# Kernel tuning notes

Measured on AMD Instinct MI355X. Metric: run time of the kernel, lower is better.

Reference implementation:

```python
import jax, jax.numpy as jnp
import numpy as np

N = 65536          # nodes
K = 12             # graph_k
CHUNK = 1024       # graph_knn_chunk (capped at 1024 in source)
WIDTH = 256        # mlp width
GWIDTH = 192       # graph width
DEPTH = 7          # mlp depth
GLAYERS = 4        # graph layers
COND = 64          # cond_dim
NUM_FF = 8         # fourier num per sigma
SIGMAS = (1.0, 10.0, 50.0)
SKIPS = (3, 6)     # residual skips
OUT_SCALE = 0.01
FF_DIM = 2 * len(SIGMAS) * NUM_FF  # 48 (sin+cos per sigma band)


def fourier_feats(x, B):
    # x: (N,3), B: (S,3,NUM_FF) -> (N, 2*S*NUM_FF)
    proj = jnp.einsum('nd,sdm->nsm', x, B).reshape(x.shape[0], -1)
    return jnp.concatenate([jnp.sin(proj), jnp.cos(proj)], axis=-1)


def knn_graph(x):
    # chunked exact kNN: mirrors _build_knn_graph (chunked cdist + top-k)
    x_sq = jnp.sum(x * x, axis=1)  # (N,)
    n = x.shape[0]
    col_ids = jnp.arange(n)

    def chunk_fn(start):
        rows = start + jnp.arange(CHUNK)
        xc = x[rows]                                   # (C,3)
        d = x_sq[rows][:, None] + x_sq[None, :] - 2.0 * (xc @ x.T)  # (C,N)
        d = jnp.maximum(d, 0.0)
        d = d + jnp.where(rows[:, None] == col_ids[None, :], 1e9, 0.0)  # exclude self
        _, idx = jax.lax.top_k(-d, K)                  # k smallest distances
        return idx

    idx = jax.lax.map(chunk_fn, jnp.arange(0, n, CHUNK))  # (n/C, C, K)
    return idx.reshape(n, K)


def setup_inputs() -> dict:
    key = jax.random.key(0)
    ks = jax.random.split(key, 16)
    g = lambda k, shape, fan: jax.random.normal(k, shape, jnp.float32) / np.sqrt(fan)
    sig = jnp.asarray(SIGMAS, jnp.float32)[:, None, None]
    return {
        'x': jax.random.normal(ks[0], (N, 3), jnp.float32),
        'cond': jax.random.normal(ks[1], (COND,), jnp.float32),
        'B': jax.random.normal(ks[2], (len(SIGMAS), 3, NUM_FF), jnp.float32) * sig,
        'W_in': g(ks[3], (FF_DIM, WIDTH), FF_DIM),
        'b_in': jnp.zeros((WIDTH,), jnp.float32),
        'Wg_in': g(ks[4], (FF_DIM, GWIDTH), FF_DIM),
        'bg_in': jnp.zeros((GWIDTH,), jnp.float32),
        'Ws': g(ks[5], (GLAYERS, GWIDTH, GWIDTH), GWIDTH),
        'Wn': g(ks[6], (GLAYERS, GWIDTH, GWIDTH), GWIDTH),
        'bg': jnp.zeros((GLAYERS, GWIDTH), jnp.float32),
        'Wg_out': g(ks[7], (GWIDTH, WIDTH), GWIDTH),
        'W': g(ks[8], (DEPTH, WIDTH, WIDTH), WIDTH),
        'bmlp': jnp.zeros((DEPTH, WIDTH), jnp.float32),
        'Wf_g': g(ks[9], (DEPTH, COND, WIDTH), COND),
        'bf_g': jnp.zeros((DEPTH, WIDTH), jnp.float32),
        'Wf_b': g(ks[10], (DEPTH, COND, WIDTH), COND),
        'bf_b': jnp.zeros((DEPTH, WIDTH), jnp.float32),
        'W_out': g(ks[11], (WIDTH, 3), WIDTH),
        'b_out': jnp.zeros((3,), jnp.float32),
    }


def reference(x, cond, B, W_in, b_in, Wg_in, bg_in, Ws, Wn, bg, Wg_out,
              W, bmlp, Wf_g, bf_g, Wf_b, bf_b, W_out, b_out):
    act = jax.nn.silu
    knn_idx = knn_graph(x)                     # (N,K) graph structure
    ff = fourier_feats(x, B)                   # (N,48)
    h0 = act(ff @ W_in + b_in)                 # (N,256) coordinate embedding

    # graph message-passing branch (row-normalized 1/K adjacency == neighbor mean)
    gfeat = act(ff @ Wg_in + bg_in)            # (N,192)
    for l in range(GLAYERS):
        agg = jnp.mean(gfeat[knn_idx], axis=1)  # sparse spmm: gather + mean
        gfeat = act(gfeat @ Ws[l] + agg @ Wn[l] + bg[l])

    h = h0 + gfeat @ Wg_out                    # inject graph context

    # FiLM-conditioned residual MLP trunk
    for l in range(DEPTH):
        gamma = cond @ Wf_g[l] + bf_g[l]       # (256,)
        beta = cond @ Wf_b[l] + bf_b[l]
        h = act((h @ W[l] + bmlp[l]) * (1.0 + gamma) + beta)
        if (l + 1) in SKIPS:
            h = h + h0

    return (h @ W_out + b_out) * OUT_SCALE     # (N,3) displacement
```

## Files before the change

kernel.cpp:

```cpp
#include <hip/hip_runtime.h>
#include <math.h>

#define NN      65536
#define KNN     12
#define WIDTH   256
#define GW      192
#define DEPTH   7
#define GLAYERS 4
#define FF      48

#define GC    192
#define GC3   7077888
#define GLO   (-6.0f)
#define GCW   0.0625f
#define GINV  16.0f

#define GS     128
#define GS3    2097152
#define GSINV  10.666666667f
#define CS2    0.09375f

#define QL    16

#define RT2   0.2025f

typedef __attribute__((ext_vector_type(8))) _Float16 half8;
typedef __attribute__((ext_vector_type(4))) _Float16 half4;
typedef __attribute__((ext_vector_type(4))) float    f4;

__device__ __forceinline__ float silu_f(float v) { return v / (1.0f + expf(-v)); }

#define KSWAP(A,B,IA,IB) do { if (B < A) { float _t=A; A=B; B=_t; int _u=IA; IA=IB; IB=_u; } } while(0)
#define KINSERT(DV,IV) do { b11=(DV); j11=(IV); \
    KSWAP(b10,b11,j10,j11); KSWAP(b9,b10,j9,j10); KSWAP(b8,b9,j8,j9); \
    KSWAP(b7,b8,j7,j8);  KSWAP(b6,b7,j6,j7);  KSWAP(b5,b6,j5,j6); \
    KSWAP(b4,b5,j4,j5);  KSWAP(b3,b4,j3,j4);  KSWAP(b2,b3,j2,j3); \
    KSWAP(b1,b2,j1,j2);  KSWAP(b0,b1,j0,j1); } while(0)

__device__ __forceinline__ int cell_of(float v) {
    int c = (int)floorf((v - GLO) * GINV);
    return min(max(c, 0), GC-1);
}

__device__ __forceinline__ int cell2(float v) {
    int c = (int)floorf((v - GLO) * GSINV);
    return min(max(c, 0), GS-1);
}

__global__ __launch_bounds__(256) void zero_both_kernel(int* __restrict__ cnt,
                                                        int* __restrict__ cnt2,
                                                        int* __restrict__ octr) {
    int g = blockIdx.x*256 + threadIdx.x;
    if (g == 0) { octr[0] = 0; octr[1] = 0; octr[2] = 0; }
    if (g < GC3/4) *(int4*)&cnt[g*4] = make_int4(0,0,0,0);
    else           *(int4*)&cnt2[(g - GC3/4)*4] = make_int4(0,0,0,0);
}

__global__ __launch_bounds__(256) void prep_hist_kernel(const float* __restrict__ x,
                                                        float4* __restrict__ xw,
                                                        int* __restrict__ cnt,
                                                        int* __restrict__ cnt2) {
    int i = blockIdx.x*256 + threadIdx.x;
    float a = x[3*i], b = x[3*i+1], c = x[3*i+2];
    xw[i] = make_float4(a, b, c, a*a + b*b + c*c);
    atomicAdd(&cnt[(cell_of(c)*GC + cell_of(b))*GC + cell_of(a)], 1);
    atomicAdd(&cnt2[(cell2(c)*GS + cell2(b))*GS + cell2(a)], 1);
}

__global__ __launch_bounds__(256) void satx_kernel(int* __restrict__ S) {
    const int wid  = (blockIdx.x*256 + threadIdx.x) >> 6;
    const int lane = threadIdx.x & 63;
    const int base = wid * GC;
    int carry = 0;
#pragma unroll
    for (int seg = 0; seg < 3; ++seg) {
        int v = S[base + seg*64 + lane];
#pragma unroll
        for (int off = 1; off < 64; off <<= 1) {
            int n = __shfl_up(v, off);
            if (lane >= off) v += n;
        }
        v += carry;
        S[base + seg*64 + lane] = v;
        carry = __shfl(v, 63);
    }
}

__global__ __launch_bounds__(256) void saty_kernel(int* __restrict__ S) {
    int t = blockIdx.x*256 + threadIdx.x;
    int z = t / GC, xx = t % GC, run = 0;
    for (int y = 0; y < GC; ++y) { int idx = (z*GC + y)*GC + xx; run += S[idx]; S[idx] = run; }
}
__global__ __launch_bounds__(256) void satz_kernel(int* __restrict__ S) {
    int t = blockIdx.x*256 + threadIdx.x;
    int y = t / GC, xx = t % GC, run = 0;
    for (int z = 0; z < GC; ++z) { int idx = (z*GC + y)*GC + xx; run += S[idx]; S[idx] = run; }
}

__device__ __forceinline__ int satv(const int* __restrict__ S, int xx, int y, int z) {
    if (xx < 0 || y < 0 || z < 0) return 0;
    return S[(z*GC + y)*GC + xx];
}

__global__ __launch_bounds__(256) void seed_kernel(const float4* __restrict__ xw,
                                                   const int* __restrict__ S,
                                                   float* __restrict__ seed) {
    int q = blockIdx.x*256 + threadIdx.x;
    float4 me = xw[q];
    int cx = cell_of(me.x), cy = cell_of(me.y), cz = cell_of(me.z);

    auto boxcount = [&](int R) {
        int x0 = max(cx-R, 0), x1 = min(cx+R, GC-1);
        int y0 = max(cy-R, 0), y1 = min(cy+R, GC-1);
        int z0 = max(cz-R, 0), z1 = min(cz+R, GC-1);
        return satv(S,x1,y1,z1) - satv(S,x0-1,y1,z1) - satv(S,x1,y0-1,z1) - satv(S,x1,y1,z0-1)
             + satv(S,x0-1,y0-1,z1) + satv(S,x0-1,y1,z0-1) + satv(S,x1,y0-1,z0-1)
             - satv(S,x0-1,y0-1,z0-1);
    };

    int Rlo = 0, Rhi = 1;
    int c = boxcount(1);
    while (c < KNN + 1) {
        if (Rhi >= GC - 1) break;
        Rlo = Rhi;
        Rhi = min(Rhi << 1, GC - 1);
        c = boxcount(Rhi);
    }
    if (c < KNN + 1) { seed[q] = 3e38f; return; }
    while (Rlo + 1 < Rhi) {
        int Rm = (Rlo + Rhi) >> 1;
        if (boxcount(Rm) >= KNN + 1) Rhi = Rm; else Rlo = Rm;
    }
    const int R = Rhi;
    int x0 = max(cx-R, 0), x1 = min(cx+R, GC-1);
    int y0 = max(cy-R, 0), y1 = min(cy+R, GC-1);
    int z0 = max(cz-R, 0), z1 = min(cz+R, GC-1);
    float dx = fmaxf(me.x - (GLO + x0*GCW), (GLO + (x1+1)*GCW) - me.x);
    float dy = fmaxf(me.y - (GLO + y0*GCW), (GLO + (y1+1)*GCW) - me.y);
    float dz = fmaxf(me.z - (GLO + z0*GCW), (GLO + (z1+1)*GCW) - me.z);
    seed[q] = (dx*dx + dy*dy + dz*dz) * 1.00002f + 1e-6f;
}

__global__ __launch_bounds__(256) void scan1_kernel(const int* __restrict__ cnt,
                                                    int* __restrict__ bsum) {
    __shared__ int red[256];
    const int t = threadIdx.x;
    int4 v = ((const int4*)cnt)[blockIdx.x*256 + t];
    red[t] = v.x + v.y + v.z + v.w;
    __syncthreads();
    for (int off = 128; off > 0; off >>= 1) {
        if (t < off) red[t] += red[t + off];
        __syncthreads();
    }
    if (t == 0) bsum[blockIdx.x] = red[0];
}

__global__ __launch_bounds__(256) void scan2_kernel(int* __restrict__ bsum) {
    __shared__ int red[256];
    const int t = threadIdx.x;
    int v[8]; int s = 0;
#pragma unroll
    for (int i = 0; i < 8; ++i) { v[i] = bsum[t*8 + i]; s += v[i]; }
    red[t] = s;
    __syncthreads();
    for (int off = 1; off < 256; off <<= 1) {
        int x = (t >= off) ? red[t - off] : 0;
        __syncthreads();
        red[t] += x;
        __syncthreads();
    }
    int run = red[t] - s;
#pragma unroll
    for (int i = 0; i < 8; ++i) { int c = v[i]; bsum[t*8 + i] = run; run += c; }
}

__global__ __launch_bounds__(256) void scan3_kernel(int* __restrict__ cnt,
                                                    const int* __restrict__ bsum) {
    __shared__ int red[256];
    const int t = threadIdx.x;
    int4 v = ((const int4*)cnt)[blockIdx.x*256 + t];
    int s = v.x + v.y + v.z + v.w;
    red[t] = s;
    __syncthreads();
    for (int off = 1; off < 256; off <<= 1) {
        int x = (t >= off) ? red[t - off] : 0;
        __syncthreads();
        red[t] += x;
        __syncthreads();
    }
    int run = bsum[blockIdx.x] + red[t] - s;
    int4 o;
    o.x = run; run += v.x;
    o.y = run; run += v.y;
    o.z = run; run += v.z;
    o.w = run;
    ((int4*)cnt)[blockIdx.x*256 + t] = o;
}

__global__ __launch_bounds__(256) void scatter_kernel(const float4* __restrict__ xw,
                                                      int* __restrict__ cstart,
                                                      float4* __restrict__ sxw,
                                                      int* __restrict__ sid) {
    int i = blockIdx.x*256 + threadIdx.x;
    float4 p = xw[i];
    int cid = (cell2(p.z)*GS + cell2(p.y))*GS + cell2(p.x);
    int pos = atomicAdd(&cstart[cid], 1);
    sxw[pos] = p;
    sid[pos] = i;
}

__global__ __launch_bounds__(256) void place_kernel(const int* __restrict__ sid,
                                                    const float* __restrict__ seed,
                                                    int* __restrict__ octr,
                                                    int* __restrict__ qperm) {
    int p = blockIdx.x*256 + threadIdx.x;
    int slot;
    if (seed[sid[p]] > RT2) slot = atomicAdd(&octr[1], 1);
    else                    slot = NN - 1 - atomicAdd(&octr[2], 1);
    qperm[slot] = p;
}

#define MROUND(M) do { \
    float pb0=__shfl_xor(b0,M), pb1=__shfl_xor(b1,M), pb2=__shfl_xor(b2,M), \
          pb3=__shfl_xor(b3,M), pb4=__shfl_xor(b4,M), pb5=__shfl_xor(b5,M), \
          pb6=__shfl_xor(b6,M), pb7=__shfl_xor(b7,M), pb8=__shfl_xor(b8,M), \
          pb9=__shfl_xor(b9,M), pb10=__shfl_xor(b10,M), pb11=__shfl_xor(b11,M); \
    int  pj0=__shfl_xor(j0,M), pj1=__shfl_xor(j1,M), pj2=__shfl_xor(j2,M), \
         pj3=__shfl_xor(j3,M), pj4=__shfl_xor(j4,M), pj5=__shfl_xor(j5,M), \
         pj6=__shfl_xor(j6,M), pj7=__shfl_xor(j7,M), pj8=__shfl_xor(j8,M), \
         pj9=__shfl_xor(j9,M), pj10=__shfl_xor(j10,M), pj11=__shfl_xor(j11,M); \
    if (pb0  < b11) KINSERT(pb0, pj0);   if (pb1  < b11) KINSERT(pb1, pj1); \
    if (pb2  < b11) KINSERT(pb2, pj2);   if (pb3  < b11) KINSERT(pb3, pj3); \
    if (pb4  < b11) KINSERT(pb4, pj4);   if (pb5  < b11) KINSERT(pb5, pj5); \
    if (pb6  < b11) KINSERT(pb6, pj6);   if (pb7  < b11) KINSERT(pb7, pj7); \
    if (pb8  < b11) KINSERT(pb8, pj8);   if (pb9  < b11) KINSERT(pb9, pj9); \
    if (pb10 < b11) KINSERT(pb10, pj10); if (pb11 < b11) KINSERT(pb11, pj11); \
} while(0)

__global__ __launch_bounds__(256) void knn_direct_kernel(const float4* __restrict__ sxw,
                                                         const int* __restrict__ sid,
                                                         const int* __restrict__ cend,
                                                         const float* __restrict__ seed,
                                                         const int* __restrict__ qperm,
                                                         unsigned short* __restrict__ knn_idx) {
    const int gtid = blockIdx.x*256 + threadIdx.x;
    const int p   = qperm[gtid >> 4];
    const int sub = gtid & (QL-1);
    const float4 me = sxw[p];
    const float qsq = me.w;
    const float rr = seed[sid[p]] + 1e-3f;
    const float r = sqrtf(rr);
    const int y0 = cell2(me.y - r), y1 = cell2(me.y + r);
    const int z0 = cell2(me.z - r), z1 = cell2(me.z + r);
    const int Wy = y1 - y0 + 1;
    const int NZ = z1 - z0 + 1;

    float b0=3e38f,b1=3e38f,b2=3e38f,b3=3e38f,b4=3e38f,b5=3e38f,
          b6=3e38f,b7=3e38f,b8=3e38f,b9=3e38f,b10=3e38f,b11=3e38f;
    int   j0=-1,j1=-1,j2=-1,j3=-1,j4=-1,j5=-1,j6=-1,j7=-1,j8=-1,j9=-1,j10=-1,j11=-1;

    int zi = sub / Wy;
    int yi = sub - zi*Wy;
    const int zstep = QL / Wy;
    const int ystep = QL - zstep*Wy;

    auto rowspan = [&](int zi_, int yi_, int& t0, int& te) {
        t0 = 0; te = 0;
        if (zi_ < NZ) {
            int zz = z0 + zi_, yy = y0 + yi_;
            float ylo = (yy == 0)    ? -1e30f : GLO + yy*CS2;
            float yhi = (yy == GS-1) ?  1e30f : GLO + (yy+1)*CS2;
            float dy = fmaxf(0.0f, fmaxf(ylo - me.y, me.y - yhi));
            float zlo = (zz == 0)    ? -1e30f : GLO + zz*CS2;
            float zhi = (zz == GS-1) ?  1e30f : GLO + (zz+1)*CS2;
            float dz = fmaxf(0.0f, fmaxf(zlo - me.z, me.z - zhi));
            float rbl = fminf(rr, b11 * 1.00002f + 1e-6f);
            float rem = rbl - dy*dy - dz*dz;
            if (rem > 0.0f) {
                float xr = sqrtf(rem);
                int xl = cell2(me.x - xr), xh = cell2(me.x + xr);
                int crow = (zz*GS + yy)*GS;
                int c0 = crow + xl;
                t0 = c0 ? cend[c0-1] : 0;
                te = cend[crow + xh];
            }
        }
    };

    int t0c, tec;
    rowspan(zi, yi, t0c, tec);
    while (zi < NZ) {
        int ziN = zi + zstep, yiN = yi + ystep;
        if (yiN >= Wy) { yiN -= Wy; ++ziN; }
        int t0n, ten;
        rowspan(ziN, yiN, t0n, ten);
        for (int t = t0c; t < tec; ++t) {
            float4 c = sxw[t];
            float dot = me.x*c.x + me.y*c.y + me.z*c.z;
            float d = fmaf(-2.0f, dot, qsq + c.w);
            d = fmaxf(d, 0.0f);
            if (d < rr && d < b11 && t != p) KINSERT(d, t);
        }
        zi = ziN; yi = yiN; t0c = t0n; tec = ten;
    }
    MROUND(1); MROUND(2); MROUND(4); MROUND(8);
    if (sub == 0) {
        knn_idx[p*KNN+0]=(unsigned short)j0;  knn_idx[p*KNN+1]=(unsigned short)j1;
        knn_idx[p*KNN+2]=(unsigned short)j2;  knn_idx[p*KNN+3]=(unsigned short)j3;
        knn_idx[p*KNN+4]=(unsigned short)j4;  knn_idx[p*KNN+5]=(unsigned short)j5;
        knn_idx[p*KNN+6]=(unsigned short)j6;  knn_idx[p*KNN+7]=(unsigned short)j7;
        knn_idx[p*KNN+8]=(unsigned short)j8;  knn_idx[p*KNN+9]=(unsigned short)j9;
        knn_idx[p*KNN+10]=(unsigned short)j10; knn_idx[p*KNN+11]=(unsigned short)j11;
    }
}

__global__ __launch_bounds__(256) void convert_Wt_kernel(const float* __restrict__ W,
                                                         _Float16* __restrict__ Wt) {
    int e = blockIdx.x*256 + threadIdx.x;
    int l = e >> 16, r = e & 65535;
    int n = r >> 8, k = r & 255;
    Wt[(size_t)l*65536 + n*256 + k] = (_Float16)W[(size_t)l*65536 + k*256 + n];
}

__global__ __launch_bounds__(256) void convert_Bg_kernel(const float* __restrict__ Ws,
                                                         const float* __restrict__ Wn,
                                                         _Float16* __restrict__ Bg) {
    int e = blockIdx.x*256 + threadIdx.x;
    int l = e / 73728, r = e % 73728;
    int n = r / 384, k = r % 384;
    float v = (k < 192) ? Ws[(size_t)l*36864 + k*192 + n]
                        : Wn[(size_t)l*36864 + (k-192)*192 + n];
    Bg[(size_t)l*73728 + (size_t)n*384 + k] = (_Float16)v;
}

__global__ __launch_bounds__(256) void convert_Wgo_kernel(const float* __restrict__ Wg_out,
                                                          _Float16* __restrict__ Wgo) {
    int e = blockIdx.x*256 + threadIdx.x;
    int n = e / 192, k = e % 192;
    Wgo[e] = (_Float16)Wg_out[k*256 + n];
}

__global__ __launch_bounds__(256) void convert_Win_kernel(const float* __restrict__ W_in,
                                                          const float* __restrict__ Wg_in,
                                                          _Float16* __restrict__ WinT,
                                                          _Float16* __restrict__ WginT) {
    int e = blockIdx.x*256 + threadIdx.x;
    if (e < 16384) {
        int n = e >> 6, k = e & 63;
        WinT[e] = (_Float16)(k < FF ? W_in[k*WIDTH + n] : 0.0f);
    } else {
        int e2 = e - 16384;
        int n = e2 >> 6, k = e2 & 63;
        WginT[e2] = (_Float16)(k < FF ? Wg_in[k*GW + n] : 0.0f);
    }
}

__global__ __launch_bounds__(256) void ff_kernel(const float4* __restrict__ sxw,
                                                 const float* __restrict__ Bf,
                                                 _Float16* __restrict__ fft) {
    const int n = blockIdx.x * 256 + threadIdx.x;
    const float4 pos = sxw[n];
    const float x0 = pos.x, x1 = pos.y, x2 = pos.z;
    _Float16 v[64];
#pragma unroll
    for (int sm = 0; sm < 24; ++sm) {
        int s = sm >> 3, m = sm & 7;
        float p = x0*Bf[s*24 + m] + x1*Bf[s*24 + 8 + m] + x2*Bf[s*24 + 16 + m];
        float sv, cv; sincosf(p, &sv, &cv);
        v[sm] = (_Float16)sv; v[24 + sm] = (_Float16)cv;
    }
#pragma unroll
    for (int k = 48; k < 64; ++k) v[k] = (_Float16)0.0f;
#pragma unroll
    for (int k8 = 0; k8 < 8; ++k8)
        *(half8*)&fft[(size_t)n*64 + k8*8] = *(half8*)&v[k8*8];
}

__global__ __launch_bounds__(192) void gather_mean_kernel(const _Float16* __restrict__ g,
                                                          const unsigned short* __restrict__ idx,
                                                          _Float16* __restrict__ agg) {
    __shared__ unsigned short nb[8][KNN];
    const int t = threadIdx.x;
    const int nb8 = blockIdx.x * 8;
    if (t < 96) { int nn = t / 12, kk = t - nn*12; nb[nn][kk] = idx[(nb8+nn)*KNN + kk]; }
    __syncthreads();
    const int nloc = t / 24, c8 = t % 24;
    float acc[8] = {0,0,0,0,0,0,0,0};
#pragma unroll
    for (int k = 0; k < KNN; ++k) {
        half8 v = *(const half8*)&g[(size_t)nb[nloc][k]*GW + c8*8];
#pragma unroll
        for (int u = 0; u < 8; ++u) acc[u] += (float)v[u];
    }
    half8 o;
#pragma unroll
    for (int u = 0; u < 8; ++u) o[u] = (_Float16)(acc[u] * (1.0f/12.0f));
    *(half8*)&agg[(size_t)(nb8 + nloc)*GW + c8*8] = o;
}

__global__ __launch_bounds__(256) void film_kernel(const float* __restrict__ cond,
                                                   const float* __restrict__ Wf_g,
                                                   const float* __restrict__ bf_g,
                                                   const float* __restrict__ Wf_b,
                                                   const float* __restrict__ bf_b,
                                                   float* __restrict__ film) {
    const int l = blockIdx.x, j = threadIdx.x;
    float g = bf_g[l*WIDTH + j], b = bf_b[l*WIDTH + j];
    for (int c = 0; c < 64; ++c) {
        float cv = cond[c];
        g = fmaf(cv, Wf_g[(size_t)(l*64 + c)*WIDTH + j], g);
        b = fmaf(cv, Wf_b[(size_t)(l*64 + c)*WIDTH + j], b);
    }
    film[l*2*WIDTH + j]         = 1.0f + g;
    film[l*2*WIDTH + WIDTH + j] = b;
}

template<int EPI>
__global__ __launch_bounds__(256) void gemm_mfma(
    const _Float16* __restrict__ A1, const _Float16* __restrict__ A2,
    const _Float16* __restrict__ Bt, int K1, int Ktot, int NC,
    const float* __restrict__ bias, const float* __restrict__ film,
    const _Float16* __restrict__ h0, _Float16* __restrict__ C, int addSkip) {
    __shared__ _Float16 As[128*40];
    __shared__ _Float16 Bs[64*40];
    const int tid = threadIdx.x;
    const int bm = blockIdx.x * 128, bn = blockIdx.y * 64;
    const int wid = tid >> 6, lane = tid & 63;
    const int wm = (wid & 1) * 64, wn = (wid >> 1) * 32;
    const int m16 = lane & 15, kq = lane >> 4;
    const int ar = tid >> 1, ah = tid & 1;
    const int br = tid >> 2, bq = tid & 3;
    f4 acc[4][2];
#pragma unroll
    for (int i = 0; i < 4; ++i)
#pragma unroll
        for (int j = 0; j < 2; ++j) acc[i][j] = (f4){0.f, 0.f, 0.f, 0.f};

    for (int kc = 0; kc < Ktot; kc += 32) {
        const _Float16* Asrc; int kl, ldA;
        if (kc < K1) { Asrc = A1; kl = kc;      ldA = K1; }
        else         { Asrc = A2; kl = kc - K1; ldA = Ktot - K1; }
        {
            const float4* src = (const float4*)&Asrc[(size_t)(bm + ar)*ldA + kl + ah*16];
            *(float4*)&As[ar*40 + ah*16]     = src[0];
            *(float4*)&As[ar*40 + ah*16 + 8] = src[1];
        }
        *(float4*)&Bs[br*40 + bq*8] = *(const float4*)&Bt[(size_t)(bn + br)*Ktot + kc + bq*8];
        __syncthreads();
        half8 af[4], bf[2];
#pragma unroll
        for (int mt = 0; mt < 4; ++mt) af[mt] = *(half8*)&As[(wm + mt*16 + m16)*40 + kq*8];
#pragma unroll
        for (int nt = 0; nt < 2; ++nt) bf[nt] = *(half8*)&Bs[(wn + nt*16 + m16)*40 + kq*8];
#pragma unroll
        for (int mt = 0; mt < 4; ++mt)
#pragma unroll
            for (int nt = 0; nt < 2; ++nt)
                acc[mt][nt] = __builtin_amdgcn_mfma_f32_16x16x32_f16(af[mt], bf[nt], acc[mt][nt], 0, 0, 0);
        __syncthreads();
    }

#pragma unroll
    for (int mt = 0; mt < 4; ++mt) {
#pragma unroll
        for (int nt = 0; nt < 2; ++nt) {
            int col = bn + wn + nt*16 + m16;
#pragma unroll
            for (int r = 0; r < 4; ++r) {
                int row = bm + wm + mt*16 + kq*4 + r;
                float v = acc[mt][nt][r];
                if (EPI == 0) {
                    v = silu_f(v + bias[col]);
                } else if (EPI == 1) {
                    v = fmaf(v + bias[col], film[col], film[NC + col]);
                    v = silu_f(v);
                    if (addSkip) v += (float)h0[(size_t)row*NC + col];
                } else {
                    v += (float)h0[(size_t)row*NC + col];
                }
                C[(size_t)row*NC + col] = (_Float16)v;
            }
        }
    }
}

__global__ __launch_bounds__(256) void out_kernel(const _Float16* __restrict__ h,
                                                  const int* __restrict__ sid,
                                                  const float* __restrict__ W_out,
                                                  const float* __restrict__ b_out,
                                                  float* __restrict__ out) {
    const int n = blockIdx.x * 256 + threadIdx.x;
    float a0 = 0.f, a1 = 0.f, a2 = 0.f;
#pragma unroll 4
    for (int k8 = 0; k8 < WIDTH/8; ++k8) {
        half8 v = *(const half8*)&h[(size_t)n*WIDTH + k8*8];
#pragma unroll
        for (int u = 0; u < 8; ++u) {
            float f = (float)v[u]; int k = k8*8 + u;
            a0 = fmaf(f, W_out[k*3+0], a0);
            a1 = fmaf(f, W_out[k*3+1], a1);
            a2 = fmaf(f, W_out[k*3+2], a2);
        }
    }
    const int o = sid[n];
    out[o*3+0] = (a0 + b_out[0]) * 0.01f;
    out[o*3+1] = (a1 + b_out[1]) * 0.01f;
    out[o*3+2] = (a2 + b_out[2]) * 0.01f;
}

extern "C" void kernel_launch(void* const* d_in, const int* in_sizes, int n_in,
                              void* d_out, int out_size, void* d_ws, size_t ws_size,
                              hipStream_t stream) {
    const float* x      = (const float*)d_in[0];
    const float* cond   = (const float*)d_in[1];
    const float* Bf     = (const float*)d_in[2];
    const float* W_in   = (const float*)d_in[3];
    const float* b_in   = (const float*)d_in[4];
    const float* Wg_in  = (const float*)d_in[5];
    const float* bg_in  = (const float*)d_in[6];
    const float* Ws     = (const float*)d_in[7];
    const float* Wn     = (const float*)d_in[8];
    const float* bg     = (const float*)d_in[9];
    const float* Wg_out = (const float*)d_in[10];
    const float* W      = (const float*)d_in[11];
    const float* bmlp   = (const float*)d_in[12];
    const float* Wf_g   = (const float*)d_in[13];
    const float* bf_g   = (const float*)d_in[14];
    const float* Wf_b   = (const float*)d_in[15];
    const float* bf_b   = (const float*)d_in[16];
    const float* W_out  = (const float*)d_in[17];
    const float* b_out  = (const float*)d_in[18];
    float* out = (float*)d_out;

    char* ws = (char*)d_ws;
    unsigned short* knn_idx = (unsigned short*)(ws + 0);
    int*       sid     = (int*)      (ws + 1572864);
    int*       qperm   = (int*)      (ws + 1835008);
    int*       octr    = (int*)      (ws + 2097152);
    float4*    xw      = (float4*)   (ws + 3145728);
    _Float16*  WinT    = (_Float16*) (ws + 3145728);
    _Float16*  WginT   = (_Float16*) (ws + 3178496);
    float*     film    = (float*)    (ws + 4194304);
    _Float16*  Bg_t    = (_Float16*) (ws + 4210688);
    _Float16*  Wgo_t   = (_Float16*) (ws + 4800512);
    _Float16*  Wt      = (_Float16*) (ws + 4898816);
    _Float16*  h0      = (_Float16*) (ws + 5816320);
    int*       cnt     = (int*)      (ws + 5816320);
    float*     seed    = (float*)    (ws + 34127872);
    _Float16*  g_a     = (_Float16*) (ws + 39370752);
    int*       cellCnt = (int*)      (ws + 39370752);
    int*       bsum    = (int*)      (ws + 47759360);
    float4*    sxw     = (float4*)   (ws + 47767552);
    _Float16*  g_b     = (_Float16*) (ws + 64536576);
    _Float16*  agg     = (_Float16*) (ws + 89702400);
    _Float16*  hA      = (_Float16*) (ws + 114868224);
    _Float16*  hB      = (_Float16*) (ws + 148422656);
    _Float16*  fft     = (_Float16*) (ws + 148422656);

    zero_both_kernel<<<(GC3+GS3)/1024, 256, 0, stream>>>(cnt, cellCnt, octr);
    prep_hist_kernel<<<NN/256, 256, 0, stream>>>(x, xw, cnt, cellCnt);
    satx_kernel<<<GC*GC/4, 256, 0, stream>>>(cnt);
    saty_kernel<<<GC*GC/256, 256, 0, stream>>>(cnt);
    satz_kernel<<<GC*GC/256, 256, 0, stream>>>(cnt);
    seed_kernel<<<NN/256, 256, 0, stream>>>(xw, cnt, seed);

    scan1_kernel<<<GS3/1024, 256, 0, stream>>>(cellCnt, bsum);
    scan2_kernel<<<1, 256, 0, stream>>>(bsum);
    scan3_kernel<<<GS3/1024, 256, 0, stream>>>(cellCnt, bsum);
    scatter_kernel<<<NN/256, 256, 0, stream>>>(xw, cellCnt, sxw, sid);
    place_kernel<<<NN/256, 256, 0, stream>>>(sid, seed, octr, qperm);
    knn_direct_kernel<<<NN*QL/256, 256, 0, stream>>>(sxw, sid, cellCnt, seed, qperm, knn_idx);

    film_kernel<<<DEPTH, 256, 0, stream>>>(cond, Wf_g, bf_g, Wf_b, bf_b, film);
    convert_Wt_kernel<<<DEPTH*65536/256, 256, 0, stream>>>(W, Wt);
    convert_Bg_kernel<<<GLAYERS*73728/256, 256, 0, stream>>>(Ws, Wn, Bg_t);
    convert_Wgo_kernel<<<256*192/256, 256, 0, stream>>>(Wg_out, Wgo_t);
    convert_Win_kernel<<<28672/256, 256, 0, stream>>>(W_in, Wg_in, WinT, WginT);
    ff_kernel<<<NN/256, 256, 0, stream>>>(sxw, Bf, fft);
    gemm_mfma<0><<<dim3(NN/128, WIDTH/64), 256, 0, stream>>>(
        fft, nullptr, WinT, 64, 64, WIDTH, b_in, nullptr, nullptr, h0, 0);
    gemm_mfma<0><<<dim3(NN/128, GW/64), 256, 0, stream>>>(
        fft, nullptr, WginT, 64, 64, GW, bg_in, nullptr, nullptr, g_a, 0);

    _Float16* gin = g_a; _Float16* gout = g_b;
    for (int l = 0; l < GLAYERS; ++l) {
        gather_mean_kernel<<<NN/8, 192, 0, stream>>>(gin, knn_idx, agg);
        gemm_mfma<0><<<dim3(NN/128, GW/64), 256, 0, stream>>>(
            gin, agg, Bg_t + (size_t)l*73728, GW, 2*GW, GW,
            bg + l*GW, nullptr, nullptr, gout, 0);
        _Float16* t = gin; gin = gout; gout = t;
    }
    gemm_mfma<2><<<dim3(NN/128, WIDTH/64), 256, 0, stream>>>(
        gin, nullptr, Wgo_t, GW, GW, WIDTH, nullptr, nullptr, h0, hA, 0);

    _Float16* hin = hA; _Float16* hout = hB;
    for (int l = 0; l < DEPTH; ++l) {
        int skip = (l == 2 || l == 5) ? 1 : 0;
        gemm_mfma<1><<<dim3(NN/128, WIDTH/64), 256, 0, stream>>>(
            hin, nullptr, Wt + (size_t)l*65536, WIDTH, WIDTH, WIDTH,
            bmlp + l*WIDTH, film + l*2*WIDTH, h0, hout, skip);
        _Float16* t = hin; hin = hout; hout = t;
    }
    out_kernel<<<NN/256, 256, 0, stream>>>(hin, sid, W_out, b_out, out);
}
```

Measured before the change: 928.2 us.

## Fuse the seven FiLM MLP trunk layers into one persistent-tile kernel

Replaces the seven per-layer GEMM launches of the MLP trunk with one kernel. Each block keeps a 128-row activation tile in registers and LDS across all layers and streams each layer's weights through LDS in 64-column chunks. This removes the global-memory round trip of the 65536x256 activations between layers and six kernel launches. The cost is heavy LDS use (about 100KB), which limits occupancy, plus reloading the weights per block and serialised syncs with no prefetch.

```diff
diff --git a/kernel.cpp b/kernel.cpp
--- a/kernel.cpp
+++ b/kernel.cpp
@@ -23,6 +23,8 @@
 #define QL    16
 
 #define RT2   0.2025f
+
+#define TSTRIDE 264
 
 typedef __attribute__((ext_vector_type(8))) _Float16 half8;
 typedef __attribute__((ext_vector_type(4))) _Float16 half4;
@@ -481,6 +483,92 @@
                 C[(size_t)row*NC + col] = (_Float16)v;
             }
         }
+    }
+}
+
+__global__ __launch_bounds__(256) void trunk_fused_kernel(
+    const _Float16* __restrict__ hA, const _Float16* __restrict__ Wt,
+    const float* __restrict__ bmlp, const float* __restrict__ film,
+    const _Float16* __restrict__ h0, _Float16* __restrict__ hOut) {
+    __shared__ _Float16 act[4*32*TSTRIDE];
+    __shared__ _Float16 Bs[64*TSTRIDE];
+    const int tid = threadIdx.x;
+    const int wv = tid >> 6, lane = tid & 63;
+    const int m16 = lane & 15, kq = lane >> 4;
+    const int wsl = wv * 32 * TSTRIDE;
+    const int brow = blockIdx.x * 128 + wv * 32;
+
+    half8 af[2][8];
+#pragma unroll
+    for (int mt = 0; mt < 2; ++mt)
+#pragma unroll
+        for (int kc = 0; kc < 8; ++kc)
+            af[mt][kc] = *(const half8*)&hA[(size_t)(brow + mt*16 + m16)*WIDTH + kc*32 + kq*8];
+
+    for (int l = 0; l < DEPTH; ++l) {
+        const _Float16* Wl = Wt + (size_t)l*65536;
+        const float* fg = film + l*2*WIDTH;
+        const float* bb = bmlp + l*WIDTH;
+        const int skip = (l == 2 || l == 5);
+#pragma unroll
+        for (int nc = 0; nc < 4; ++nc) {
+            __syncthreads();
+#pragma unroll
+            for (int j = 0; j < 8; ++j) {
+                int jj = tid + j*256;
+                int row = jj >> 5, k8 = jj & 31;
+                *(float4*)&Bs[row*TSTRIDE + k8*8] =
+                    *(const float4*)&Wl[(size_t)(nc*64 + row)*WIDTH + k8*8];
+            }
+            __syncthreads();
+            f4 acc[2][4];
+#pragma unroll
+            for (int mt = 0; mt < 2; ++mt)
+#pragma unroll
+                for (int nt = 0; nt < 4; ++nt) acc[mt][nt] = (f4){0.f,0.f,0.f,0.f};
+#pragma unroll
+            for (int kc = 0; kc < 8; ++kc) {
+                half8 bf[4];
+#pragma unroll
+                for (int nt = 0; nt < 4; ++nt)
+                    bf[nt] = *(half8*)&Bs[(nt*16 + m16)*TSTRIDE + kc*32 + kq*8];
+#pragma unroll
+                for (int mt = 0; mt < 2; ++mt)
+#pragma unroll
+                    for (int nt = 0; nt < 4; ++nt)
+                        acc[mt][nt] = __builtin_amdgcn_mfma_f32_16x16x32_f16(
+                            af[mt][kc], bf[nt], acc[mt][nt], 0, 0, 0);
+            }
+#pragma unroll
+            for (int mt = 0; mt < 2; ++mt)
+#pragma unroll
+                for (int nt = 0; nt < 4; ++nt) {
+                    int col = nc*64 + nt*16 + m16;
+                    float ga = fg[col], be = fg[WIDTH + col], bi = bb[col];
+#pragma unroll
+                    for (int r = 0; r < 4; ++r) {
+                        int lrow = mt*16 + kq*4 + r;
+                        float v = fmaf(acc[mt][nt][r] + bi, ga, be);
+                        v = silu_f(v);
+                        if (skip) v += (float)h0[(size_t)(brow + lrow)*WIDTH + col];
+                        act[wsl + lrow*TSTRIDE + col] = (_Float16)v;
+                    }
+                }
+        }
+        if (l < DEPTH-1) {
+#pragma unroll
+            for (int mt = 0; mt < 2; ++mt)
+#pragma unroll
+                for (int kc = 0; kc < 8; ++kc)
+                    af[mt][kc] = *(half8*)&act[wsl + (mt*16 + m16)*TSTRIDE + kc*32 + kq*8];
+        }
+    }
+#pragma unroll
+    for (int j = 0; j < 16; ++j) {
+        int jj = lane + j*64;
+        int row = jj >> 5, k8 = jj & 31;
+        *(float4*)&hOut[(size_t)(brow + row)*WIDTH + k8*8] =
+            *(float4*)&act[wsl + row*TSTRIDE + k8*8];
     }
 }
 
@@ -593,13 +681,7 @@
     gemm_mfma<2><<<dim3(NN/128, WIDTH/64), 256, 0, stream>>>(
         gin, nullptr, Wgo_t, GW, GW, WIDTH, nullptr, nullptr, h0, hA, 0);
 
-    _Float16* hin = hA; _Float16* hout = hB;
-    for (int l = 0; l < DEPTH; ++l) {
-        int skip = (l == 2 || l == 5) ? 1 : 0;
-        gemm_mfma<1><<<dim3(NN/128, WIDTH/64), 256, 0, stream>>>(
-            hin, nullptr, Wt + (size_t)l*65536, WIDTH, WIDTH, WIDTH,
-            bmlp + l*WIDTH, film + l*2*WIDTH, h0, hout, skip);
-        _Float16* t = hin; hin = hout; hout = t;
-    }
-    out_kernel<<<NN/256, 256, 0, stream>>>(hin, sid, W_out, b_out, out);
-}
+    trunk_fused_kernel<<<NN/128, 256, 0, stream>>>(hA, Wt, bmlp, film, h0, hB);
+
+    out_kernel<<<NN/256, 256, 0, stream>>>(hB, sid, W_out, b_out, out);
+}
```

Result: slower. 1.004 ms (+8.1%).
